# Kernel optimization log

Measured on AMD Instinct MI355X. Metric: run time of the kernel, lower is better.

Reference implementation:

```python
import math
import jax, jax.numpy as jnp
import numpy as np

EMBED_DIM = 512
NUM_HEADS = 8
EDGE_VOC = 16
EDGE_PAD = 0
L, B = 512, 16


def setup_inputs() -> dict:
    key = jax.random.key(0)
    ks = jax.random.split(key, 8)
    x = jax.random.normal(ks[0], (L, B, EMBED_DIM), dtype=jnp.float32)
    edge = jax.random.randint(ks[1], (B, L, L), 0, EDGE_VOC, dtype=jnp.int32)
    key_padding_mask = jnp.zeros((B, L), dtype=bool)
    # causal additive mask, as from nn.Transformer.generate_square_subsequent_mask
    attn_mask = jnp.where(jnp.triu(jnp.ones((L, L), bool), k=1), -jnp.inf, 0.0).astype(jnp.float32)
    s = 1.0 / math.sqrt(EMBED_DIM)
    in_proj_w = jax.random.uniform(ks[2], (3 * EMBED_DIM, EMBED_DIM), jnp.float32, -s, s)
    in_proj_b = jnp.zeros((3 * EMBED_DIM,), jnp.float32)
    out_proj_w = jax.random.uniform(ks[3], (EMBED_DIM, EMBED_DIM), jnp.float32, -s, s)
    out_proj_b = jnp.zeros((EMBED_DIM,), jnp.float32)
    edge_emb = jax.random.normal(ks[4], (EDGE_VOC, NUM_HEADS), dtype=jnp.float32)
    edge_emb = edge_emb.at[EDGE_PAD].set(0.0)  # padding_idx row zeroed
    return {"x": x, "edge": edge, "key_padding_mask": key_padding_mask,
            "attn_mask": attn_mask, "in_proj_w": in_proj_w, "in_proj_b": in_proj_b,
            "out_proj_w": out_proj_w, "out_proj_b": out_proj_b, "edge_emb": edge_emb}


def reference(x, edge, key_padding_mask, attn_mask,
              in_proj_w, in_proj_b, out_proj_w, out_proj_b, edge_emb):
    length, bsz, embed_dim = x.shape
    H = edge_emb.shape[1]
    hd = embed_dim // H
    qkv = x @ in_proj_w.T + in_proj_b                       # (L, B, 3E)
    q, k, v = jnp.split(qkv, 3, axis=-1)
    # (L, B*H, hd) -> (B*H, L, hd)
    q = q.reshape(length, bsz * H, hd).transpose(1, 0, 2)
    k = k.reshape(length, bsz * H, hd).transpose(1, 0, 2)
    v = v.reshape(length, bsz * H, hd).transpose(1, 0, 2)
    # combine attn_mask with key padding
    mask = attn_mask[None]                                   # (1, L, L)
    kpm = jnp.broadcast_to(key_padding_mask[:, None, None, :],
                           (bsz, H, 1, length)).reshape(bsz * H, 1, length)
    mask = jnp.where(kpm, -jnp.inf, mask)                    # (B*H, 1/L, L)
    # edge bias: (B, L, L, H) -> (B*H, L, L)
    ebias = edge_emb[edge].transpose(0, 3, 1, 2).reshape(bsz * H, length, length)
    q = q / math.sqrt(hd)
    scores = jnp.einsum('bqd,bkd->bqk', q, k) + mask + ebias
    attn = jax.nn.softmax(scores, axis=-1)
    out = jnp.einsum('bqk,bkd->bqd', attn, v)                # (B*H, L, hd)
    out = out.transpose(1, 0, 2).reshape(length, bsz, embed_dim)
    return out @ out_proj_w.T + out_proj_b
```

## Files before the change

### kernel.cpp

```cpp
#include <hip/hip_runtime.h>
#include <hip/hip_bf16.h>


typedef __attribute__((ext_vector_type(8))) short bf16x8;
typedef __attribute__((ext_vector_type(4))) float f32x4;
typedef __attribute__((ext_vector_type(4))) int i32x4;
typedef __attribute__((ext_vector_type(4))) unsigned int u32x4;

#define LOG2E 1.44269504088896340736f
#define QK_SCALE 0.18033688011112042f

__device__ inline void gll16(const void* g, const void* l) {
  __builtin_amdgcn_global_load_lds(
      (const __attribute__((address_space(1))) unsigned int*)g,
      (__attribute__((address_space(3))) unsigned int*)l, 16, 0, 0);
}

__device__ inline short f2bf(float x) {
  __hip_bfloat16 t = __float2bfloat16(x);
  return *reinterpret_cast<short*>(&t);
}

__device__ inline void cstore(__hip_bfloat16* C, size_t idx, float v) {
  C[idx] = __float2bfloat16(v);
}
__device__ inline void cstore(float* C, size_t idx, float v) { C[idx] = v; }

__global__ void cvt3(const float* __restrict__ x, const float* __restrict__ w1,
                     const float* __restrict__ w2, const int* __restrict__ edge,
                     __hip_bfloat16* __restrict__ xb,
                     __hip_bfloat16* __restrict__ w1b,
                     __hip_bfloat16* __restrict__ w2b,
                     unsigned char* __restrict__ epk) {
  const int blk = blockIdx.x;
  const int tid = threadIdx.x;
  if (blk >= 2560) {
    __shared__ unsigned char Ls[4 * 512];
    const int pblk = blk - 2560;
    const int b = pblk >> 7;
    const int q0 = (pblk & 127) * 4;
    const int row = tid >> 6, lk = tid & 63;
    const int k0 = lk * 8;
    const int* src = edge + ((size_t)(b * 512 + q0 + row)) * 512 + k0;
    const i32x4 a = *(const i32x4*)src;
    const i32x4 b4 = *(const i32x4*)(src + 4);
    const unsigned int lo =
        (unsigned)a[0] | ((unsigned)a[1] << 8) | ((unsigned)a[2] << 16) |
        ((unsigned)a[3] << 24);
    const unsigned int hi =
        (unsigned)b4[0] | ((unsigned)b4[1] << 8) | ((unsigned)b4[2] << 16) |
        ((unsigned)b4[3] << 24);
    const int kt = k0 >> 6, kk = k0 & 63;
    const int mt = kk >> 4, quad = (kk >> 2) & 3;
    const int doff = row * 512 + kt * 64 + quad * 16 + mt * 4;
    *(unsigned int*)&Ls[doff] = lo;
    *(unsigned int*)&Ls[doff + 16] = hi;
    __syncthreads();
    const int okt = tid >> 5, rowi = (tid >> 3) & 3, off8 = (tid & 7) * 8;
    const unsigned long long v =
        *(const unsigned long long*)&Ls[rowi * 512 + okt * 64 + off8];
    *(unsigned long long*)&epk[(((size_t)(b * 8 + okt) * 512) + q0 + rowi) *
                                   64 +
                               off8] = v;
    return;
  }
  const float* src;
  __hip_bfloat16* dst;
  int off;
  if (blk < 2048)      { src = x;  dst = xb;  off = blk; }
  else if (blk < 2432) { src = w1; dst = w1b; off = blk - 2048; }
  else                 { src = w2; dst = w2b; off = blk - 2432; }
  const int i = (off * 256 + tid) * 8;
  const float4 a = *(const float4*)(src + i);
  const float4 b = *(const float4*)(src + i + 4);
  bf16x8 r;
  r[0] = f2bf(a.x); r[1] = f2bf(a.y); r[2] = f2bf(a.z); r[3] = f2bf(a.w);
  r[4] = f2bf(b.x); r[5] = f2bf(b.y); r[6] = f2bf(b.z); r[7] = f2bf(b.w);
  *(bf16x8*)(dst + i) = r;
}

template <int MT, int RB, typename TC, bool QS = false, bool BROW = false>
__global__ __launch_bounds__(256, RB) void gemm_bt(
    const __hip_bfloat16* __restrict__ A,
    const __hip_bfloat16* __restrict__ W,
    const float* __restrict__ bias,
    TC* __restrict__ C, int N, int K) {
  constexpr int MI = MT / 32;
  __shared__ short As[MT * 32];
  __shared__ short Ws[128 * 32];
  const int tid = threadIdx.x;
  const int wave = tid >> 6, lane = tid & 63;
  const int c = lane & 15, quad = lane >> 4;
  const int nb = N >> 7;
  const int bx = blockIdx.x % nb, by = blockIdx.x / nb;
  const int m0 = by * MT, n0 = bx << 7;
  const int wm = wave >> 1, wn = wave & 1;

  f32x4 acc[MI][4] = {};
  const int ar = lane >> 2;
  const int ak = (lane & 3) * 8;

  for (int k0 = 0; k0 < K; k0 += 32) {
    __syncthreads();
#pragma unroll
    for (int i = 0; i < MT / 64; i++) {
      const int r0 = i * 64 + wave * 16;
      gll16(A + (size_t)(m0 + r0 + ar) * K + k0 + ak, &As[r0 * 32]);
    }
#pragma unroll
    for (int i = 0; i < 2; i++) {
      const int r0 = i * 64 + wave * 16;
      gll16(W + (size_t)(n0 + r0 + ar) * K + k0 + ak, &Ws[r0 * 32]);
    }
    __syncthreads();
    bf16x8 af[MI], bfr[4];
#pragma unroll
    for (int i = 0; i < MI; i++)
      af[i] = *(const bf16x8*)&As[(wm * (MT / 2) + i * 16 + c) * 32 + quad * 8];
#pragma unroll
    for (int j = 0; j < 4; j++)
      bfr[j] = *(const bf16x8*)&Ws[(wn * 64 + j * 16 + c) * 32 + quad * 8];
#pragma unroll
    for (int i = 0; i < MI; i++)
#pragma unroll
      for (int j = 0; j < 4; j++)
        acc[i][j] = __builtin_amdgcn_mfma_f32_16x16x32_bf16(af[i], bfr[j],
                                                            acc[i][j], 0, 0, 0);
  }
#pragma unroll
  for (int j = 0; j < 4; j++) {
    const int col = n0 + wn * 64 + j * 16 + c;
    const float bv = bias[col];
#pragma unroll
    for (int i = 0; i < MI; i++) {
      const int row = m0 + wm * (MT / 2) + i * 16 + quad * 4;
#pragma unroll
      for (int r = 0; r < 4; r++) {
        float v = acc[i][j][r] + bv;
        if constexpr (QS) {
          if (col < 512) v *= QK_SCALE;
        }
        int orow = row + r;
        if constexpr (BROW) orow = ((orow & 15) << 9) | (orow >> 4);
        cstore(C, (size_t)orow * N + col, v);
      }
    }
  }
}

__global__ __launch_bounds__(256, 4) void attn_kernel(
    const __hip_bfloat16* __restrict__ qkv,
    const unsigned char* __restrict__ epk,
    const float* __restrict__ edge_emb,
    __hip_bfloat16* __restrict__ attn_out) {
  __shared__ short Ks[2][64 * 72];
  __shared__ short Vt[2][64 * 72];
  __shared__ float eeS[16];

  const int tid = threadIdx.x;
  const int wave = tid >> 6, lane = tid & 63;
  const int c = lane & 15, quad = lane >> 4;
  const int i = blockIdx.x;
  const int xcd = i & 7;
  const int j = i >> 3;
  const int pr = j & 3;
  const int h = (j >> 2) & 7;
  const int b = xcd + ((j >> 5) << 3);
  const int colq = h * 64;

  if (tid < 16) eeS[tid] = (edge_emb[tid * 8 + h] - 16.0f) * LOG2E;

  const int r2 = tid >> 3;
  const int cc = (tid & 7) * 8;
  const int kcol0 = ((r2 << 1) & 7) | (((r2 >> 2) ^ (cc >> 3)) << 3);
  const size_t sbase0 = (size_t)(b * 512 + r2 * 2) * 1536 + colq + cc;

#pragma unroll
  for (int sidx = 0; sidx < 2; sidx++) {
    const int qb = sidx ? (7 - pr) : pr;
    const int nkt = qb + 1;
    const int q_g = (qb << 6) + wave * 16 + c;
    bf16x8 qf0, qf1;
    {
      const __hip_bfloat16* qp_ = qkv + (size_t)(b * 512 + q_g) * 1536 + colq;
      qf0 = *(const bf16x8*)(qp_ + quad * 8);
      qf1 = *(const bf16x8*)(qp_ + 32 + quad * 8);
    }
    float lsum = 0.f;
    f32x4 o[4] = {};
    const unsigned char* eb =
        epk + (((size_t)(b * 8) * 512 + q_g) << 6) + (quad << 4);
    bf16x8 kreg[2], vreg[2];
    kreg[0] = *(const bf16x8*)(qkv + sbase0 + 512);
    vreg[0] = *(const bf16x8*)(qkv + sbase0 + 1024);
    kreg[1] = *(const bf16x8*)(qkv + sbase0 + 1536 + 512);
    vreg[1] = *(const bf16x8*)(qkv + sbase0 + 1536 + 1024);

    if (sidx) __syncthreads();

    for (int kt = 0; kt < nkt; kt++) {
      const bool last = (kt == qb);
      const int mtmax = last ? (wave + 1) : 4;
      const int cur = kt & 1;
      *(bf16x8*)&Ks[cur][(r2 * 2) * 72 + cc] = kreg[0];
      *(bf16x8*)&Ks[cur][(r2 * 2 + 1) * 72 + cc] = kreg[1];
#pragma unroll
      for (int j2 = 0; j2 < 8; j2++) {
        short2 p;
        p.x = vreg[0][j2];
        p.y = vreg[1][j2];
        *(short2*)&Vt[cur][(cc + j2) * 72 + kcol0] = p;
      }
      if (kt + 1 < nkt) {
        const size_t nb_ = sbase0 + (size_t)(kt + 1) * 64 * 1536;
        kreg[0] = *(const bf16x8*)(qkv + nb_ + 512);
        vreg[0] = *(const bf16x8*)(qkv + nb_ + 1024);
        kreg[1] = *(const bf16x8*)(qkv + nb_ + 1536 + 512);
        vreg[1] = *(const bf16x8*)(qkv + nb_ + 1536 + 1024);
      }
      const i32x4 e16 = *(const i32x4*)(eb + ((size_t)kt << 15));
      __syncthreads();

      f32x4 st[4];
      __builtin_amdgcn_s_setprio(1);
#pragma unroll
      for (int mt = 0; mt < 4; mt++) {
        if (mt >= mtmax) continue;
        const unsigned int w = (unsigned int)e16[mt];
        f32x4 z;
#pragma unroll
        for (int r = 0; r < 4; r++) z[r] = eeS[(w >> (8 * r)) & 15];
        const bf16x8 ka =
            *(const bf16x8*)&Ks[cur][(mt * 16 + c) * 72 + quad * 8];
        const bf16x8 kb =
            *(const bf16x8*)&Ks[cur][(mt * 16 + c) * 72 + 32 + quad * 8];
        z = __builtin_amdgcn_mfma_f32_16x16x32_bf16(ka, qf0, z, 0, 0, 0);
        st[mt] = __builtin_amdgcn_mfma_f32_16x16x32_bf16(kb, qf1, z, 0, 0, 0);
      }
      __builtin_amdgcn_s_setprio(0);

      unsigned int wp[4][2];
      float rs[4] = {0.f, 0.f, 0.f, 0.f};
#pragma unroll
      for (int mt = 0; mt < 4; mt++) {
        if (mt < mtmax) {
          float pv[4];
          if (last && mt == wave) {
#pragma unroll
            for (int r = 0; r < 4; r++) {
              pv[r] = (quad * 4 + r <= c) ? exp2f(st[mt][r]) : 0.0f;
              rs[r] += pv[r];
            }
          } else {
#pragma unroll
            for (int r = 0; r < 4; r++) {
              pv[r] = exp2f(st[mt][r]);
              rs[r] += pv[r];
            }
          }
          asm("v_cvt_pk_bf16_f32 %0, %1, %2"
              : "=v"(wp[mt][0]) : "v"(pv[0]), "v"(pv[1]));
          asm("v_cvt_pk_bf16_f32 %0, %1, %2"
              : "=v"(wp[mt][1]) : "v"(pv[2]), "v"(pv[3]));
        } else {
          wp[mt][0] = 0u;
          wp[mt][1] = 0u;
        }
      }
      lsum += (rs[0] + rs[1]) + (rs[2] + rs[3]);

      const bool skip_hi = last && (wave < 2);
      u32x4 paw;
      {
        unsigned int a0 = wp[0][0], b0 = wp[1][0];
        asm("v_permlane32_swap_b32 %0, %1" : "+v"(a0), "+v"(b0));
        asm("v_permlane16_swap_b32 %0, %1" : "+v"(a0), "+v"(b0));
        unsigned int a1 = wp[0][1], b1 = wp[1][1];
        asm("v_permlane32_swap_b32 %0, %1" : "+v"(a1), "+v"(b1));
        asm("v_permlane16_swap_b32 %0, %1" : "+v"(a1), "+v"(b1));
        paw[0] = a0; paw[1] = a1; paw[2] = b0; paw[3] = b1;
      }
      const bf16x8 pa0 = *(const bf16x8*)&paw;
      bf16x8 pa1;
      if (!skip_hi) {
        u32x4 pbw;
        unsigned int a0 = wp[2][0], b0 = wp[3][0];
        asm("v_permlane32_swap_b32 %0, %1" : "+v"(a0), "+v"(b0));
        asm("v_permlane16_swap_b32 %0, %1" : "+v"(a0), "+v"(b0));
        unsigned int a1 = wp[2][1], b1 = wp[3][1];
        asm("v_permlane32_swap_b32 %0, %1" : "+v"(a1), "+v"(b1));
        asm("v_permlane16_swap_b32 %0, %1" : "+v"(a1), "+v"(b1));
        pbw[0] = a0; pbw[1] = a1; pbw[2] = b0; pbw[3] = b1;
        pa1 = *(const bf16x8*)&pbw;
      }

      __builtin_amdgcn_s_setprio(1);
#pragma unroll
      for (int nt = 0; nt < 4; nt++) {
        const int n = nt * 16 + c;
        const bf16x8 vb0 =
            *(const bf16x8*)&Vt[cur][n * 72 + ((quad ^ (n >> 3)) << 3)];
        o[nt] =
            __builtin_amdgcn_mfma_f32_16x16x32_bf16(pa0, vb0, o[nt], 0, 0, 0);
        if (!skip_hi) {
          const bf16x8 vb1 =
              *(const bf16x8*)&Vt[cur][n * 72 + (((4 + quad) ^ (n >> 3)) << 3)];
          o[nt] =
              __builtin_amdgcn_mfma_f32_16x16x32_bf16(pa1, vb1, o[nt], 0, 0, 0);
        }
      }
      __builtin_amdgcn_s_setprio(0);
    }

    float l = lsum;
    l += __shfl_xor(l, 16);
    l += __shfl_xor(l, 32);
    float lr[4];
#pragma unroll
    for (int r = 0; r < 4; r++) lr[r] = __shfl(l, quad * 4 + r, 16);
    const int qrow0 = (qb << 6) + wave * 16 + quad * 4;
#pragma unroll
    for (int nt = 0; nt < 4; nt++)
#pragma unroll
      for (int r = 0; r < 4; r++)
        attn_out[(size_t)((qrow0 + r) * 16 + b) * 512 + colq + nt * 16 + c] =
            __float2bfloat16(o[nt][r] / lr[r]);
  }
}

extern "C" void kernel_launch(void* const* d_in, const int* in_sizes, int n_in,
                              void* d_out, int out_size, void* d_ws, size_t ws_size,
                              hipStream_t stream) {
  const float* x    = (const float*)d_in[0];
  const int* edge   = (const int*)d_in[1];
  const float* ipw  = (const float*)d_in[4];
  const float* ipb  = (const float*)d_in[5];
  const float* opw  = (const float*)d_in[6];
  const float* opb  = (const float*)d_in[7];
  const float* eemb = (const float*)d_in[8];
  float* out = (float*)d_out;

  __hip_bfloat16* qkv  = (__hip_bfloat16*)d_ws;
  __hip_bfloat16* attn = qkv + (size_t)8192 * 1536;
  __hip_bfloat16* xb   = attn + (size_t)8192 * 512;
  __hip_bfloat16* w1b  = xb + (size_t)8192 * 512;
  __hip_bfloat16* w2b  = w1b + (size_t)1536 * 512;
  unsigned char* epk = (unsigned char*)(w2b + (size_t)512 * 512);

  cvt3<<<4608, 256, 0, stream>>>(x, ipw, opw, edge, xb, w1b, w2b, epk);
  gemm_bt<128, 3, __hip_bfloat16, true, true>
      <<<768, 256, 0, stream>>>(xb, w1b, ipb, qkv, 1536, 512);
  attn_kernel<<<512, 256, 0, stream>>>(qkv, epk, eemb, attn);
  gemm_bt<64, 2, float>
      <<<512, 256, 0, stream>>>(attn, w2b, opb, out, 512, 512);
}
```

Baseline: 146.5 us.

## Move edge packing and out-proj weight conversion into QKV GEMM launch

The edge-index byte packing and out_proj weight bf16 conversion move out of the first conversion kernel and into extra blocks of a new fused QKV GEMM kernel. The conversion kernel now only converts x and in_proj weights. The aim is to shorten the serial conversion stage and let the memory-bound edge packing run alongside the compute-bound GEMM tiles. In exchange, the GEMM launch grows, and the packing blocks come first in block order, so they may hold CUs ahead of the GEMM tiles.

```diff
diff --git a/kernel.cpp b/kernel.cpp
--- a/kernel.cpp
+++ b/kernel.cpp
@@ -27,18 +27,42 @@
 __device__ inline void cstore(float* C, size_t idx, float v) { C[idx] = v; }
 
 __global__ void cvt3(const float* __restrict__ x, const float* __restrict__ w1,
-                     const float* __restrict__ w2, const int* __restrict__ edge,
                      __hip_bfloat16* __restrict__ xb,
-                     __hip_bfloat16* __restrict__ w1b,
-                     __hip_bfloat16* __restrict__ w2b,
-                     unsigned char* __restrict__ epk) {
+                     __hip_bfloat16* __restrict__ w1b) {
   const int blk = blockIdx.x;
   const int tid = threadIdx.x;
-  if (blk >= 2560) {
-    __shared__ unsigned char Ls[4 * 512];
-    const int pblk = blk - 2560;
-    const int b = pblk >> 7;
-    const int q0 = (pblk & 127) * 4;
+  const float* src;
+  __hip_bfloat16* dst;
+  int off;
+  if (blk < 2048) { src = x;  dst = xb;  off = blk; }
+  else            { src = w1; dst = w1b; off = blk - 2048; }
+  const int i = (off * 256 + tid) * 8;
+  const float4 a = *(const float4*)(src + i);
+  const float4 b = *(const float4*)(src + i + 4);
+  bf16x8 r;
+  r[0] = f2bf(a.x); r[1] = f2bf(a.y); r[2] = f2bf(a.z); r[3] = f2bf(a.w);
+  r[4] = f2bf(b.x); r[5] = f2bf(b.y); r[6] = f2bf(b.z); r[7] = f2bf(b.w);
+  *(bf16x8*)(dst + i) = r;
+}
+
+__global__ __launch_bounds__(256, 3) void gemm1_fused(
+    const __hip_bfloat16* __restrict__ A,
+    const __hip_bfloat16* __restrict__ W,
+    const float* __restrict__ bias,
+    __hip_bfloat16* __restrict__ C,
+    const int* __restrict__ edge,
+    const float* __restrict__ w2,
+    unsigned char* __restrict__ epk,
+    __hip_bfloat16* __restrict__ w2b) {
+  __shared__ __align__(16) short As[128 * 32];
+  __shared__ short Ws[128 * 32];
+  const int blk = blockIdx.x;
+  const int tid = threadIdx.x;
+
+  if (blk < 2048) {
+    unsigned char* Ls = (unsigned char*)As;
+    const int b = blk >> 7;
+    const int q0 = (blk & 127) * 4;
     const int row = tid >> 6, lk = tid & 63;
     const int k0 = lk * 8;
     const int* src = edge + ((size_t)(b * 512 + q0 + row)) * 512 + k0;
@@ -64,22 +88,70 @@
                                off8] = v;
     return;
   }
-  const float* src;
-  __hip_bfloat16* dst;
-  int off;
-  if (blk < 2048)      { src = x;  dst = xb;  off = blk; }
-  else if (blk < 2432) { src = w1; dst = w1b; off = blk - 2048; }
-  else                 { src = w2; dst = w2b; off = blk - 2432; }
-  const int i = (off * 256 + tid) * 8;
-  const float4 a = *(const float4*)(src + i);
-  const float4 b = *(const float4*)(src + i + 4);
-  bf16x8 r;
-  r[0] = f2bf(a.x); r[1] = f2bf(a.y); r[2] = f2bf(a.z); r[3] = f2bf(a.w);
-  r[4] = f2bf(b.x); r[5] = f2bf(b.y); r[6] = f2bf(b.z); r[7] = f2bf(b.w);
-  *(bf16x8*)(dst + i) = r;
-}
-
-template <int MT, int RB, typename TC, bool QS = false, bool BROW = false>
+  if (blk < 2176) {
+    const int i = ((blk - 2048) * 256 + tid) * 8;
+    const float4 a = *(const float4*)(w2 + i);
+    const float4 b = *(const float4*)(w2 + i + 4);
+    bf16x8 r;
+    r[0] = f2bf(a.x); r[1] = f2bf(a.y); r[2] = f2bf(a.z); r[3] = f2bf(a.w);
+    r[4] = f2bf(b.x); r[5] = f2bf(b.y); r[6] = f2bf(b.z); r[7] = f2bf(b.w);
+    *(bf16x8*)(w2b + i) = r;
+    return;
+  }
+
+  const int gblk = blk - 2176;
+  const int wave = tid >> 6, lane = tid & 63;
+  const int c = lane & 15, quad = lane >> 4;
+  const int bx = gblk % 12, by = gblk / 12;
+  const int m0 = by * 128, n0 = bx << 7;
+  const int wm = wave >> 1, wn = wave & 1;
+
+  f32x4 acc[4][4] = {};
+  const int ar = lane >> 2;
+  const int ak = (lane & 3) * 8;
+
+  for (int k0 = 0; k0 < 512; k0 += 32) {
+    __syncthreads();
+#pragma unroll
+    for (int i = 0; i < 2; i++) {
+      const int r0 = i * 64 + wave * 16;
+      gll16(A + (size_t)(m0 + r0 + ar) * 512 + k0 + ak, &As[r0 * 32]);
+      gll16(W + (size_t)(n0 + r0 + ar) * 512 + k0 + ak, &Ws[r0 * 32]);
+    }
+    __syncthreads();
+    bf16x8 af[4], bfr[4];
+#pragma unroll
+    for (int i = 0; i < 4; i++)
+      af[i] = *(const bf16x8*)&As[(wm * 64 + i * 16 + c) * 32 + quad * 8];
+#pragma unroll
+    for (int j = 0; j < 4; j++)
+      bfr[j] = *(const bf16x8*)&Ws[(wn * 64 + j * 16 + c) * 32 + quad * 8];
+#pragma unroll
+    for (int i = 0; i < 4; i++)
+#pragma unroll
+      for (int j = 0; j < 4; j++)
+        acc[i][j] = __builtin_amdgcn_mfma_f32_16x16x32_bf16(af[i], bfr[j],
+                                                            acc[i][j], 0, 0, 0);
+  }
+#pragma unroll
+  for (int j = 0; j < 4; j++) {
+    const int col = n0 + wn * 64 + j * 16 + c;
+    const float bv = bias[col];
+    const float sc = (col < 512) ? QK_SCALE : 1.0f;
+#pragma unroll
+    for (int i = 0; i < 4; i++) {
+      const int row = m0 + wm * 64 + i * 16 + quad * 4;
+#pragma unroll
+      for (int r = 0; r < 4; r++) {
+        const float v = (acc[i][j][r] + bv) * sc;
+        const int orow = (((row + r) & 15) << 9) | ((row + r) >> 4);
+        C[(size_t)orow * 1536 + col] = __float2bfloat16(v);
+      }
+    }
+  }
+}
+
+template <int MT, int RB, typename TC>
 __global__ __launch_bounds__(256, RB) void gemm_bt(
     const __hip_bfloat16* __restrict__ A,
     const __hip_bfloat16* __restrict__ W,
@@ -135,15 +207,8 @@
     for (int i = 0; i < MI; i++) {
       const int row = m0 + wm * (MT / 2) + i * 16 + quad * 4;
 #pragma unroll
-      for (int r = 0; r < 4; r++) {
-        float v = acc[i][j][r] + bv;
-        if constexpr (QS) {
-          if (col < 512) v *= QK_SCALE;
-        }
-        int orow = row + r;
-        if constexpr (BROW) orow = ((orow & 15) << 9) | (orow >> 4);
-        cstore(C, (size_t)orow * N + col, v);
-      }
+      for (int r = 0; r < 4; r++)
+        cstore(C, (size_t)(row + r) * N + col, acc[i][j][r] + bv);
     }
   }
 }
@@ -347,9 +412,8 @@
   __hip_bfloat16* w2b  = w1b + (size_t)1536 * 512;
   unsigned char* epk = (unsigned char*)(w2b + (size_t)512 * 512);
 
-  cvt3<<<4608, 256, 0, stream>>>(x, ipw, opw, edge, xb, w1b, w2b, epk);
-  gemm_bt<128, 3, __hip_bfloat16, true, true>
-      <<<768, 256, 0, stream>>>(xb, w1b, ipb, qkv, 1536, 512);
+  cvt3<<<2432, 256, 0, stream>>>(x, ipw, xb, w1b);
+  gemm1_fused<<<2944, 256, 0, stream>>>(xb, w1b, ipb, qkv, edge, opw, epk, w2b);
   attn_kernel<<<512, 256, 0, stream>>>(qkv, epk, eemb, attn);
   gemm_bt<64, 2, float>
       <<<512, 256, 0, stream>>>(attn, w2b, opb, out, 512, 512);
```

After: 149.2 us. About the same (+1.9%).
